# Optimization experiments

Measured on AMD Instinct MI355X. Metric: run time of the kernel, lower is better.

Reference implementation:

```python
import jax, jax.numpy as jnp
import numpy as np
from jax import lax

EPSILON = 0.05      # sinkhorn entropic regularization (module init arg)
N_SINKHORN = 100    # fixed iteration count (POT default numItermax=1000 w/ early stop 1e-9)


def setup_inputs() -> dict:
    key = jax.random.key(0)
    k1, k2, k3 = jax.random.split(key, 3)
    B, D = 2048, 1024
    audio_emb = jax.random.normal(k1, (B, D), dtype=jnp.float32)
    text_emb = jax.random.normal(k2, (B, D), dtype=jnp.float32)
    # learned metric L (set via set_L); PSD so diag(L) > 0 and sqrt is real
    A = jax.random.normal(k3, (D, D), dtype=jnp.float32)
    L = (A @ A.T) / jnp.float32(D)
    return {"audio_emb": audio_emb, "text_emb": text_emb, "L": L}


def reference(audio_emb, text_emb, L):
    B = audio_emb.shape[0]
    M = jnp.nan_to_num(L)
    # SVD is computed in the original (reg term), but the final loss discards it
    s = jnp.linalg.svd(M, compute_uv=False)
    _reg = jnp.sum(s)  # unused in returned loss (original: loss = wloss)

    # einsum('ijk,ikj,kk->ij') only reads diag(M):
    # M_dist[i,j] = sum_k diag(M)[k] * (audio[j,k] - text[i,k])^2
    w = jnp.diagonal(M)  # [D]
    aw = jnp.einsum('jd,d->j', audio_emb * audio_emb, w)        # [B]
    tw = jnp.einsum('id,d->i', text_emb * text_emb, w)          # [B]
    cross = jnp.einsum('id,jd->ij', text_emb * w, audio_emb)    # [B,B]
    M_dist = tw[:, None] + aw[None, :] - 2.0 * cross
    M_dist = jnp.sqrt(jnp.maximum(M_dist, 0.0))
    M_dist = M_dist / jnp.max(M_dist)

    # Sinkhorn-Knopp (ot.sinkhorn, method='sinkhorn')
    a = jnp.ones((B,), dtype=M_dist.dtype) / B
    b = jnp.ones((B,), dtype=M_dist.dtype) / B
    K = jnp.exp(-M_dist / EPSILON)  # [B,B]

    def step(uv, _):
        u, v = uv
        v = b / (K.T @ u)
        u = a / (K @ v)
        return (u, v), None

    u0 = jnp.ones((B,), dtype=M_dist.dtype) / B
    v0 = jnp.ones((B,), dtype=M_dist.dtype) / B
    (u, v), _ = lax.scan(step, (u0, v0), None, length=N_SINKHORN)
    # pi = diag(u) K diag(v); pi_hat = eye(B)/B -> only diag(pi) matters
    pi_diag = u * jnp.diagonal(K) * v  # [B]
    wloss = -jnp.sum(jnp.log(pi_diag)) / B
    return wloss
```

## Files before the change

### kernel.cpp

```cpp
#include <hip/hip_runtime.h>
#include <hip/hip_fp16.h>
#include <math.h>

#define NB 2048
#define ND 1024
#define EPS 0.05f
#define NITER 100
#define SBLK 64
#define KSCALE 16384.0f
#define LOG_KSCALE 9.704060527839234

typedef float f32x4 __attribute__((ext_vector_type(4)));
typedef short s16x8 __attribute__((ext_vector_type(8)));
typedef unsigned short u16x4 __attribute__((ext_vector_type(4)));
union Uh { f32x4 f; __half2 h[4]; };

__global__ void prep_k(const float* __restrict__ L, float* __restrict__ w,
                       float* __restrict__ u, float* __restrict__ v,
                       unsigned* __restrict__ maxbits, unsigned* __restrict__ flags) {
    int gtid = blockIdx.x * 256 + threadIdx.x;
    if (gtid < ND) {
        float x = L[(size_t)gtid * (ND + 1)];
        if (x != x) x = 0.f;
        else if (fabsf(x) == INFINITY) x = (x > 0.f) ? 3.4028235e38f : -3.4028235e38f;
        w[gtid] = x;
    }
    u[gtid] = 1.0f / NB;
    v[gtid] = 1.0f / NB;
    if (gtid == 0) *maxbits = 0u;
    if (gtid < 512) flags[gtid] = 0u;
}

__global__ __launch_bounds__(256) void rows_k(const float* __restrict__ audio,
                                              const float* __restrict__ text,
                                              const float* __restrict__ w,
                                              float* __restrict__ aw, float* __restrict__ tw) {
    int r = blockIdx.x, tid = threadIdx.x;
    float4 wv = *(const float4*)&w[tid * 4];
    float4 a4 = *(const float4*)&audio[(size_t)r * ND + tid * 4];
    float4 t4 = *(const float4*)&text[(size_t)r * ND + tid * 4];
    float sa = a4.x * a4.x * wv.x + a4.y * a4.y * wv.y + a4.z * a4.z * wv.z + a4.w * a4.w * wv.w;
    float st = t4.x * t4.x * wv.x + t4.y * t4.y * wv.y + t4.z * t4.z * wv.z + t4.w * t4.w * wv.w;
    #pragma unroll
    for (int off = 32; off; off >>= 1) {
        sa += __shfl_down(sa, off, 64);
        st += __shfl_down(st, off, 64);
    }
    __shared__ float red[8];
    if ((tid & 63) == 0) { red[tid >> 6] = sa; red[4 + (tid >> 6)] = st; }
    __syncthreads();
    if (tid == 0) {
        aw[r] = red[0] + red[1] + red[2] + red[3];
        tw[r] = red[4] + red[5] + red[6] + red[7];
    }
}

__device__ __forceinline__ unsigned short f2bf(float x) {
    unsigned uu = __float_as_uint(x);
    return (unsigned short)((uu + 0x7FFFu + ((uu >> 16) & 1u)) >> 16);
}

__global__ __launch_bounds__(256) void gemm_mdist(
        const float* __restrict__ Tm, const float* __restrict__ Am,
        const float* __restrict__ wd, const float* __restrict__ tw, const float* __restrict__ aw,
        __half* __restrict__ Md, __half* __restrict__ MdT,
        float* __restrict__ diagMd, unsigned* __restrict__ maxbits) {
    __shared__ __align__(16) unsigned char smem[38912];
    float* wl = (float*)(smem + 34816);
    const int t = threadIdx.x;
    const int row0 = blockIdx.y * 128, col0 = blockIdx.x * 128;
    *(f32x4*)&wl[t * 4] = *(const f32x4*)&wd[t * 4];
    const int wv = t >> 6;
    const int wr = wv >> 1, wc = wv & 1;
    const int l = t & 63, lr = l & 15, kg = l >> 4;
    const int trow = t >> 4, tk4 = t & 15;
    const int px = (((tk4 >> 1) ^ (trow & 7)) << 4) + ((tk4 & 1) << 3);
    f32x4 acc[4][4];
    #pragma unroll
    for (int m = 0; m < 4; ++m)
        #pragma unroll
        for (int n = 0; n < 4; ++n) acc[m][n] = (f32x4){0.f, 0.f, 0.f, 0.f};
    __syncthreads();
    const float* tp = Tm + (size_t)(row0 + trow) * ND + tk4 * 4;
    const float* ap = Am + (size_t)(col0 + trow) * ND + tk4 * 4;
    for (int k0 = 0; k0 < ND; k0 += 64) {
        f32x4 wv4 = *(const f32x4*)&wl[k0 + tk4 * 4];
        __syncthreads();
        #pragma unroll
        for (int s = 0; s < 8; ++s) {
            f32x4 tv = *(const f32x4*)(tp + (size_t)(s * 16) * ND + k0);
            f32x4 av = *(const f32x4*)(ap + (size_t)(s * 16) * ND + k0);
            tv *= wv4;
            u16x4 tb, ab;
            tb[0] = f2bf(tv[0]); tb[1] = f2bf(tv[1]); tb[2] = f2bf(tv[2]); tb[3] = f2bf(tv[3]);
            ab[0] = f2bf(av[0]); ab[1] = f2bf(av[1]); ab[2] = f2bf(av[2]); ab[3] = f2bf(av[3]);
            const int rb = (s * 16 + trow) * 128 + px;
            *(u16x4*)(smem + rb) = tb;
            *(u16x4*)(smem + 16384 + rb) = ab;
        }
        __syncthreads();
        #pragma unroll
        for (int kk = 0; kk < 2; ++kk) {
            const int sl = (((kk << 2) + kg) ^ (lr & 7)) << 4;
            s16x8 af[4], bfr[4];
            #pragma unroll
            for (int m = 0; m < 4; ++m)
                af[m] = *(const s16x8*)(smem + (wr * 64 + m * 16 + lr) * 128 + sl);
            #pragma unroll
            for (int n = 0; n < 4; ++n)
                bfr[n] = *(const s16x8*)(smem + 16384 + (wc * 64 + n * 16 + lr) * 128 + sl);
            #pragma unroll
            for (int m = 0; m < 4; ++m)
                #pragma unroll
                for (int n = 0; n < 4; ++n)
                    acc[m][n] = __builtin_amdgcn_mfma_f32_16x16x32_bf16(af[m], bfr[n], acc[m][n], 0, 0, 0);
        }
    }
    __syncthreads();
    unsigned short* tr = (unsigned short*)smem;
    unsigned short* mdp = (unsigned short*)Md;
    float lmax = 0.f;
    #pragma unroll
    for (int m = 0; m < 4; ++m) {
        #pragma unroll
        for (int r = 0; r < 4; ++r) {
            const int li = wr * 64 + m * 16 + kg * 4 + r;
            const int i = row0 + li;
            const float twi = tw[i];
            #pragma unroll
            for (int n = 0; n < 4; ++n) {
                const int lj = wc * 64 + n * 16 + lr;
                const int j = col0 + lj;
                float md = twi + aw[j] - 2.0f * acc[m][n][r];
                md = sqrtf(fmaxf(md, 0.f));
                lmax = fmaxf(lmax, md);
                const unsigned short hb = __half_as_ushort(__float2half(md));
                mdp[(size_t)i * NB + j] = hb;
                tr[lj * 136 + li] = hb;
                if (i == j) diagMd[i] = md;
            }
        }
    }
    __syncthreads();
    {
        const int jj = t >> 1, ih = (t & 1) * 64;
        unsigned short* dst = (unsigned short*)MdT + (size_t)(col0 + jj) * NB + row0 + ih;
        #pragma unroll
        for (int x = 0; x < 8; ++x)
            *(s16x8*)(dst + x * 8) = *(const s16x8*)&tr[jj * 136 + ih + x * 8];
    }
    #pragma unroll
    for (int off = 32; off; off >>= 1) lmax = fmaxf(lmax, __shfl_down(lmax, off, 64));
    float* red = (float*)(smem + 34816);
    if (l == 0) red[t >> 6] = lmax;
    __syncthreads();
    if (t == 0) {
        float m2 = fmaxf(fmaxf(red[0], red[1]), fmaxf(red[2], red[3]));
        atomicMax(maxbits, __float_as_uint(m2));
    }
}

__global__ __launch_bounds__(256) void expconv_k(__half* __restrict__ Kall,
                                                 const unsigned* __restrict__ maxbits) {
    const float mx = __uint_as_float(*maxbits);
    const float cc = -1.0f / (mx * EPS);
    size_t idx = ((size_t)blockIdx.x * 256 + threadIdx.x) << 3;
    Uh uu; uu.f = *(const f32x4*)(Kall + idx);
    #pragma unroll
    for (int q = 0; q < 4; ++q) {
        float2 f = __half22float2(uu.h[q]);
        f.x = __expf(f.x * cc) * KSCALE;
        f.y = __expf(f.y * cc) * KSCALE;
        uu.h[q] = __floats2half2_rn(f.x, f.y);
    }
    *(f32x4*)(Kall + idx) = uu.f;
}

__device__ __forceinline__ void wait_phase(const unsigned* __restrict__ pollp, int w, unsigned ph) {
    if (w == 0) {
        for (;;) {
            unsigned f;
            asm volatile("global_load_dword %0, %1, off sc0 sc1\n\t"
                         "s_waitcnt vmcnt(0)"
                         : "=&v"(f) : "v"(pollp) : "memory");
            if (__all(f >= ph)) break;
            __builtin_amdgcn_s_sleep(1);
        }
    }
}

__device__ __forceinline__ void stage(const float* __restrict__ src, float* sv, int tid) {
    const float* p0 = src + (tid << 2);
    f32x4 r0;
    asm volatile("global_load_dwordx4 %0, %1, off sc0 sc1\n\t"
                 "s_waitcnt vmcnt(0)"
                 : "=&v"(r0) : "v"(p0) : "memory");
    *(f32x4*)&sv[(tid << 2) + ((tid >> 1) << 2)] = r0;
}

__device__ __forceinline__ void half_step(const __half* __restrict__ Kmat,
                                          float* __restrict__ xout,
                                          const float* sv, int row0, float ab, int l) {
    float acc[4] = {0.f, 0.f, 0.f, 0.f};
    const __half* kb = Kmat + (size_t)row0 * NB;
    #pragma unroll
    for (int c = 0; c < 4; ++c) {
        const int col = (c << 9) + (l << 3);
        const int phys = col + ((col >> 3) << 2);
        f32x4 s0 = *(const f32x4*)&sv[phys];
        f32x4 s1 = *(const f32x4*)&sv[phys + 4];
        #pragma unroll
        for (int r = 0; r < 4; ++r) {
            Uh uu; uu.f = *(const f32x4*)(kb + (size_t)r * NB + col);
            float2 f0 = __half22float2(uu.h[0]);
            float2 f1 = __half22float2(uu.h[1]);
            float2 f2 = __half22float2(uu.h[2]);
            float2 f3 = __half22float2(uu.h[3]);
            acc[r] = fmaf(f0.x, s0.x, acc[r]);
            acc[r] = fmaf(f0.y, s0.y, acc[r]);
            acc[r] = fmaf(f1.x, s0.z, acc[r]);
            acc[r] = fmaf(f1.y, s0.w, acc[r]);
            acc[r] = fmaf(f2.x, s1.x, acc[r]);
            acc[r] = fmaf(f2.y, s1.y, acc[r]);
            acc[r] = fmaf(f3.x, s1.z, acc[r]);
            acc[r] = fmaf(f3.y, s1.w, acc[r]);
        }
    }
    #pragma unroll
    for (int r = 0; r < 4; ++r) {
        #pragma unroll
        for (int off = 32; off; off >>= 1) acc[r] += __shfl_down(acc[r], off, 64);
    }
    if (l == 0) {
        f32x4 o;
        o[0] = ab / acc[0]; o[1] = ab / acc[1]; o[2] = ab / acc[2]; o[3] = ab / acc[3];
        asm volatile("global_store_dwordx4 %1, %0, off sc0 sc1"
                     :: "v"(o), "v"(xout + row0) : "memory");
    }
    asm volatile("s_waitcnt vmcnt(0)" ::: "memory");
}

__global__ __launch_bounds__(512, 1) void sinkhorn_k(
        const __half* __restrict__ Kr, const __half* __restrict__ Kc,
        float* __restrict__ u, float* __restrict__ v,
        unsigned* __restrict__ flags) {
    __shared__ __align__(16) float sv[3072];
    const int tid = threadIdx.x, bid = blockIdx.x;
    const int w = tid >> 6, l = tid & 63;
    const int row0 = ((bid << 3) + w) << 2;
    const float ab = 1.0f / NB;
    unsigned* myflag = flags + (bid << 2);
    const unsigned* pollp = flags + ((l & 63) << 2);
    for (int it = 0; it < NITER; ++it) {
        wait_phase(pollp, w, 2 * it);
        __syncthreads();
        stage(u, sv, tid);
        __syncthreads();
        half_step(Kc, v, sv, row0, ab, l);
        __syncthreads();
        if (tid == 0) {
            unsigned ph = 2 * it + 1;
            asm volatile("global_store_dword %1, %0, off sc0 sc1"
                         :: "v"(ph), "v"(myflag) : "memory");
        }
        wait_phase(pollp, w, 2 * it + 1);
        __syncthreads();
        stage(v, sv, tid);
        __syncthreads();
        half_step(Kr, u, sv, row0, ab, l);
        __syncthreads();
        if (tid == 0) {
            unsigned ph = 2 * it + 2;
            asm volatile("global_store_dword %1, %0, off sc0 sc1"
                         :: "v"(ph), "v"(myflag) : "memory");
        }
    }
}

__global__ void loss_k(const float* __restrict__ u, const float* __restrict__ v,
                       const float* __restrict__ diagMd, const unsigned* __restrict__ maxbits,
                       float* __restrict__ out) {
    int tid = threadIdx.x;
    float mx = __uint_as_float(*maxbits);
    float cc = 1.0f / (mx * EPS);
    double s = 0.0;
    for (int i = tid; i < NB; i += 256)
        s += (double)(logf(u[i]) + logf(v[i]) - diagMd[i] * cc);
    #pragma unroll
    for (int off = 32; off; off >>= 1) s += __shfl_down(s, off, 64);
    __shared__ double red[4];
    if ((tid & 63) == 0) red[tid >> 6] = s;
    __syncthreads();
    if (tid == 0)
        out[0] = (float)(-(red[0] + red[1] + red[2] + red[3]) / (double)NB - LOG_KSCALE);
}

extern "C" void kernel_launch(void* const* d_in, const int* in_sizes, int n_in,
                              void* d_out, int out_size, void* d_ws, size_t ws_size,
                              hipStream_t stream) {
    const float* audio = (const float*)d_in[0];
    const float* text  = (const float*)d_in[1];
    const float* L     = (const float*)d_in[2];
    char* ws = (char*)d_ws;
    float*    w       = (float*)(ws + 0);
    float*    aw      = (float*)(ws + 4096);
    float*    tw      = (float*)(ws + 12288);
    float*    u       = (float*)(ws + 20480);
    float*    v       = (float*)(ws + 28672);
    float*    diagMd  = (float*)(ws + 36864);
    unsigned* maxbits = (unsigned*)(ws + 45056);
    unsigned* flags   = (unsigned*)(ws + 45312);
    __half*   Md      = (__half*)(ws + 65536);
    __half*   MdT     = (__half*)(ws + 65536 + (size_t)NB * NB * 2);

    prep_k<<<8, 256, 0, stream>>>(L, w, u, v, maxbits, flags);
    rows_k<<<NB, 256, 0, stream>>>(audio, text, w, aw, tw);
    gemm_mdist<<<dim3(16, 16), 256, 0, stream>>>(text, audio, w, tw, aw, Md, MdT, diagMd, maxbits);
    expconv_k<<<4096, 256, 0, stream>>>(Md, maxbits);
    sinkhorn_k<<<SBLK, 512, 0, stream>>>(Md, MdT, u, v, flags);
    loss_k<<<1, 256, 0, stream>>>(u, v, diagMd, maxbits, (float*)d_out);
}
```

Baseline: 878.4 us.

## Spread persistent Sinkhorn kernel over 256 blocks with 2 rows per wave

The persistent Sinkhorn kernel now launches 256 blocks of 256 threads instead of 64 blocks of 512. Each wave handles 2 rows instead of 4, so the matrix-vector traffic is spread across more compute units. To match, the grid barrier polls 256 flags with four loads per lane, and each thread stages 8 vector elements into shared memory. This adds more memory and bandwidth parallelism per half-step, but makes the grid-wide flag barrier wider and costlier, and needs all 256 blocks to be co-resident.

```diff
diff --git a/kernel.cpp b/kernel.cpp
--- a/kernel.cpp
+++ b/kernel.cpp
@@ -6,11 +6,12 @@
 #define ND 1024
 #define EPS 0.05f
 #define NITER 100
-#define SBLK 64
+#define SBLK 256
 #define KSCALE 16384.0f
 #define LOG_KSCALE 9.704060527839234
 
 typedef float f32x4 __attribute__((ext_vector_type(4)));
+typedef float f32x2 __attribute__((ext_vector_type(2)));
 typedef short s16x8 __attribute__((ext_vector_type(8)));
 typedef unsigned short u16x4 __attribute__((ext_vector_type(4)));
 union Uh { f32x4 f; __half2 h[4]; };
@@ -28,7 +29,7 @@
     u[gtid] = 1.0f / NB;
     v[gtid] = 1.0f / NB;
     if (gtid == 0) *maxbits = 0u;
-    if (gtid < 512) flags[gtid] = 0u;
+    if (gtid < 1024) flags[gtid] = 0u;
 }
 
 __global__ __launch_bounds__(256) void rows_k(const float* __restrict__ audio,
@@ -176,32 +177,40 @@
     *(f32x4*)(Kall + idx) = uu.f;
 }
 
-__device__ __forceinline__ void wait_phase(const unsigned* __restrict__ pollp, int w, unsigned ph) {
+__device__ __forceinline__ void wait_phase(const unsigned* __restrict__ flags, int w, int l,
+                                           unsigned ph) {
     if (w == 0) {
+        const unsigned* p = flags + (l << 2);
         for (;;) {
-            unsigned f;
-            asm volatile("global_load_dword %0, %1, off sc0 sc1\n\t"
+            unsigned f0, f1, f2, f3;
+            asm volatile("global_load_dword %0, %4, off sc0 sc1\n\t"
+                         "global_load_dword %1, %5, off sc0 sc1\n\t"
+                         "global_load_dword %2, %6, off sc0 sc1\n\t"
+                         "global_load_dword %3, %7, off sc0 sc1\n\t"
                          "s_waitcnt vmcnt(0)"
-                         : "=&v"(f) : "v"(pollp) : "memory");
-            if (__all(f >= ph)) break;
+                         : "=&v"(f0), "=&v"(f1), "=&v"(f2), "=&v"(f3)
+                         : "v"(p), "v"(p + 256), "v"(p + 512), "v"(p + 768) : "memory");
+            if (__all((f0 >= ph) && (f1 >= ph) && (f2 >= ph) && (f3 >= ph))) break;
             __builtin_amdgcn_s_sleep(1);
         }
     }
 }
 
 __device__ __forceinline__ void stage(const float* __restrict__ src, float* sv, int tid) {
-    const float* p0 = src + (tid << 2);
-    f32x4 r0;
-    asm volatile("global_load_dwordx4 %0, %1, off sc0 sc1\n\t"
+    const float* p0 = src + (tid << 3);
+    f32x4 r0, r1;
+    asm volatile("global_load_dwordx4 %0, %2, off sc0 sc1\n\t"
+                 "global_load_dwordx4 %1, %3, off sc0 sc1\n\t"
                  "s_waitcnt vmcnt(0)"
-                 : "=&v"(r0) : "v"(p0) : "memory");
-    *(f32x4*)&sv[(tid << 2) + ((tid >> 1) << 2)] = r0;
+                 : "=&v"(r0), "=&v"(r1) : "v"(p0), "v"(p0 + 4) : "memory");
+    *(f32x4*)&sv[tid * 12] = r0;
+    *(f32x4*)&sv[tid * 12 + 4] = r1;
 }
 
 __device__ __forceinline__ void half_step(const __half* __restrict__ Kmat,
                                           float* __restrict__ xout,
                                           const float* sv, int row0, float ab, int l) {
-    float acc[4] = {0.f, 0.f, 0.f, 0.f};
+    float acc[2] = {0.f, 0.f};
     const __half* kb = Kmat + (size_t)row0 * NB;
     #pragma unroll
     for (int c = 0; c < 4; ++c) {
@@ -210,7 +219,7 @@
         f32x4 s0 = *(const f32x4*)&sv[phys];
         f32x4 s1 = *(const f32x4*)&sv[phys + 4];
         #pragma unroll
-        for (int r = 0; r < 4; ++r) {
+        for (int r = 0; r < 2; ++r) {
             Uh uu; uu.f = *(const f32x4*)(kb + (size_t)r * NB + col);
             float2 f0 = __half22float2(uu.h[0]);
             float2 f1 = __half22float2(uu.h[1]);
@@ -227,32 +236,31 @@
         }
     }
     #pragma unroll
-    for (int r = 0; r < 4; ++r) {
+    for (int r = 0; r < 2; ++r) {
         #pragma unroll
         for (int off = 32; off; off >>= 1) acc[r] += __shfl_down(acc[r], off, 64);
     }
     if (l == 0) {
-        f32x4 o;
-        o[0] = ab / acc[0]; o[1] = ab / acc[1]; o[2] = ab / acc[2]; o[3] = ab / acc[3];
-        asm volatile("global_store_dwordx4 %1, %0, off sc0 sc1"
+        f32x2 o;
+        o[0] = ab / acc[0]; o[1] = ab / acc[1];
+        asm volatile("global_store_dwordx2 %1, %0, off sc0 sc1"
                      :: "v"(o), "v"(xout + row0) : "memory");
     }
     asm volatile("s_waitcnt vmcnt(0)" ::: "memory");
 }
 
-__global__ __launch_bounds__(512, 1) void sinkhorn_k(
+__global__ __launch_bounds__(256, 1) void sinkhorn_k(
         const __half* __restrict__ Kr, const __half* __restrict__ Kc,
         float* __restrict__ u, float* __restrict__ v,
         unsigned* __restrict__ flags) {
     __shared__ __align__(16) float sv[3072];
     const int tid = threadIdx.x, bid = blockIdx.x;
     const int w = tid >> 6, l = tid & 63;
-    const int row0 = ((bid << 3) + w) << 2;
+    const int row0 = (bid << 3) + (w << 1);
     const float ab = 1.0f / NB;
     unsigned* myflag = flags + (bid << 2);
-    const unsigned* pollp = flags + ((l & 63) << 2);
     for (int it = 0; it < NITER; ++it) {
-        wait_phase(pollp, w, 2 * it);
+        wait_phase(flags, w, l, 2 * it);
         __syncthreads();
         stage(u, sv, tid);
         __syncthreads();
@@ -263,7 +271,7 @@
             asm volatile("global_store_dword %1, %0, off sc0 sc1"
                          :: "v"(ph), "v"(myflag) : "memory");
         }
-        wait_phase(pollp, w, 2 * it + 1);
+        wait_phase(flags, w, l, 2 * it + 1);
         __syncthreads();
         stage(v, sv, tid);
         __syncthreads();
@@ -317,6 +325,6 @@
     rows_k<<<NB, 256, 0, stream>>>(audio, text, w, aw, tw);
     gemm_mdist<<<dim3(16, 16), 256, 0, stream>>>(text, audio, w, tw, aw, Md, MdT, diagMd, maxbits);
     expconv_k<<<4096, 256, 0, stream>>>(Md, maxbits);
-    sinkhorn_k<<<SBLK, 512, 0, stream>>>(Md, MdT, u, v, flags);
+    sinkhorn_k<<<SBLK, 256, 0, stream>>>(Md, MdT, u, v, flags);
     loss_k<<<1, 256, 0, stream>>>(u, v, diagMd, maxbits, (float*)d_out);
 }
```

New measurement: 761.3 us. 1.15x faster.
